# Kernel optimization log

Hardware: AMD Instinct MI355X
Metric: run time of the kernel (lower is better)

Reference implementation:

```python
import jax, jax.numpy as jnp
import numpy as np

B, S, D, H, HD, NF, NL, V = 16, 2048, 768, 12, 64, 32, 12, 2362
EPS = 1e-6  # fast_transformers LinearAttention eps


def _rope_tables(seq_len, dim):
    inv_freq = 1.0 / (10000.0 ** (jnp.arange(0, dim, 2, dtype=jnp.float32) / dim))
    t = jnp.arange(seq_len, dtype=jnp.float32)
    freqs = jnp.einsum('s,f->sf', t, inv_freq)
    emb = jnp.concatenate([freqs, freqs], axis=-1)[None, :, None, :]  # [1,S,1,HD]
    return jnp.cos(emb), jnp.sin(emb)


def _rot_half(x):
    x1, x2 = jnp.split(x, 2, axis=-1)
    return jnp.concatenate([-x2, x1], axis=-1)


def _ln(x, g, b):
    m = jnp.mean(x, axis=-1, keepdims=True)
    v = jnp.var(x, axis=-1, keepdims=True)
    return (x - m) / jnp.sqrt(v + 1e-5) * g + b


def setup_inputs():
    key = jax.random.key(0)
    ks = jax.random.split(key, 16)
    w = lambda k, shape: jax.random.normal(k, shape, jnp.float32) * 0.02
    return {
        'idx': jax.random.randint(ks[0], (B, S), 0, V),
        'mask': jnp.ones((B, S), jnp.int32),
        'emb': w(ks[1], (V, D)),
        'wq': w(ks[2], (NL, D, D)), 'bq': jnp.zeros((NL, D), jnp.float32),
        'wk': w(ks[3], (NL, D, D)), 'bk': jnp.zeros((NL, D), jnp.float32),
        'wv': w(ks[4], (NL, D, D)), 'bv': jnp.zeros((NL, D), jnp.float32),
        'wo': w(ks[5], (NL, D, D)), 'bo': jnp.zeros((NL, D), jnp.float32),
        'omega': jax.random.normal(ks[6], (NL, HD, NF), jnp.float32),
        'g1': jnp.ones((NL, D), jnp.float32), 'be1': jnp.zeros((NL, D), jnp.float32),
        'w1': w(ks[7], (NL, D, D)), 'c1': jnp.zeros((NL, D), jnp.float32),
        'w2': w(ks[8], (NL, D, D)), 'c2': jnp.zeros((NL, D), jnp.float32),
        'g2': jnp.ones((NL, D), jnp.float32), 'be2': jnp.zeros((NL, D), jnp.float32),
        'gf': jnp.ones((D,), jnp.float32), 'bf': jnp.zeros((D,), jnp.float32),
    }


def reference(idx, mask, emb, wq, bq, wk, bk, wv, bv, wo, bo, omega,
              g1, be1, w1, c1, w2, c2, g2, be2, gf, bf):
    x = emb[idx]                     # token embedding [B,S,D]; dropout = identity (eval)
    m = mask.astype(x.dtype)         # LengthMask from mask.sum(-1); mask is contiguous ones
    cos, sin = _rope_tables(S, HD)
    for l in range(NL):
        q = (x @ wq[l] + bq[l]).reshape(B, S, H, HD)
        k = (x @ wk[l] + bk[l]).reshape(B, S, H, HD)
        v = (x @ wv[l] + bv[l]).reshape(B, S, H, HD)
        q = q * cos + _rot_half(q) * sin
        k = k * cos + _rot_half(k) * sin
        # GeneralizedRandomFeatures: phi(x) = relu(x @ omega)
        Qf = jax.nn.relu(jnp.einsum('bshd,df->bshf', q, omega[l]))
        Kf = jax.nn.relu(jnp.einsum('bshd,df->bshf', k, omega[l])) * m[:, :, None, None]
        KV = jnp.einsum('bshf,bshd->bhfd', Kf, v)                       # [B,H,NF,HD]
        Z = 1.0 / (jnp.einsum('bshf,bhf->bsh', Qf, Kf.sum(axis=1)) + EPS)
        a = jnp.einsum('bshf,bhfd,bsh->bshd', Qf, KV, Z).reshape(B, S, D)
        x = x + (a @ wo[l] + bo[l])           # residual (dropout=identity)
        x = _ln(x, g1[l], be1[l])             # post-norm
        y = jax.nn.gelu(x @ w1[l] + c1[l], approximate=False) @ w2[l] + c2[l]
        x = _ln(x + y, g2[l], be2[l])
    return _ln(x, gf, bf)                     # final encoder LayerNorm
```

## Files before the change

kernel.cpp:

```cpp
#include <hip/hip_runtime.h>
#include <cstdint>
#include <cstddef>

typedef __bf16 bf16;
typedef __bf16 bf16x8 __attribute__((ext_vector_type(8)));
typedef __bf16 bf16x4 __attribute__((ext_vector_type(4)));
typedef float f32x4 __attribute__((ext_vector_type(4)));

#define NB 16
#define SS 2048
#define HH 12
#define NLL 12
#define MTOK (NB*SS)

#define BARRIER() do { asm volatile("" ::: "memory"); __builtin_amdgcn_s_barrier(); asm volatile("" ::: "memory"); } while (0)
#define VMCNT0()  asm volatile("s_waitcnt vmcnt(0)" ::: "memory")

__device__ __forceinline__ void load16_lds(const bf16* g, bf16* l) {
    __builtin_amdgcn_global_load_lds((const __attribute__((address_space(1))) void*)g,
                                     (__attribute__((address_space(3))) void*)l, 16, 0, 0);
}

__global__ void diag_k(float* out, float code) {
    if (threadIdx.x == 0 && blockIdx.x == 0) out[0] = code;
}

__global__ __launch_bounds__(256) void packw_k(const float* __restrict__ wq, const float* __restrict__ wk,
                                               const float* __restrict__ wv, const float* __restrict__ wo,
                                               const float* __restrict__ w1, const float* __restrict__ w2,
                                               int l, bf16* qkvT_l, bf16* oT_l, bf16* w1T_l, bf16* w2T_l) {
    __shared__ float tile[32][33];
    int which = blockIdx.z;
    const float* srcs[6] = {wq, wk, wv, wo, w1, w2};
    const float* src = srcs[which] + (size_t)l * 589824;
    bf16* dst;
    if (which < 3)       dst = qkvT_l + (size_t)which * 589824;
    else if (which == 3) dst = oT_l;
    else if (which == 4) dst = w1T_l;
    else                 dst = w2T_l;
    int tx = threadIdx.x, ty = threadIdx.y;
    int bx = blockIdx.x, by = blockIdx.y;
#pragma unroll
    for (int j = 0; j < 4; ++j)
        tile[ty + j*8][tx] = src[(size_t)(by*32 + ty + j*8) * 768 + bx*32 + tx];
    __syncthreads();
#pragma unroll
    for (int j = 0; j < 4; ++j)
        dst[(size_t)(bx*32 + ty + j*8) * 768 + by*32 + tx] = (bf16)tile[tx][ty + j*8];
}

__global__ void packb_k(const float* __restrict__ bq, const float* __restrict__ bk,
                        const float* __restrict__ bv, float* bqkv) {
    int i = blockIdx.x * 256 + threadIdx.x;
    if (i >= NLL * 2304) return;
    int l = i / 2304, c = i % 2304;
    float v = (c < 768) ? bq[l*768 + c] : (c < 1536) ? bk[l*768 + c - 768] : bv[l*768 + c - 1536];
    bqkv[i] = v;
}

__global__ void rope_k(float* cosT, float* sinT) {
    int i = blockIdx.x * 256 + threadIdx.x;
    int s = i >> 6, j = i & 63, f = j & 31;
    float inv = powf(10000.f, -(float)(2*f) * (1.0f/64.0f));
    float ang = (float)s * inv;
    cosT[i] = cosf(ang);
    sinT[i] = sinf(ang);
}

__global__ __launch_bounds__(192) void embed_k(const int* __restrict__ idx, const float* __restrict__ emb,
                                               float* __restrict__ x, bf16* __restrict__ xb) {
    size_t tok = blockIdx.x;
    int t = threadIdx.x;
    int id = idx[tok];
    float4 v = *(const float4*)&emb[(size_t)id * 768 + t*4];
    *(float4*)&x[tok * 768 + t*4] = v;
    bf16x4 o; o[0] = (bf16)v.x; o[1] = (bf16)v.y; o[2] = (bf16)v.z; o[3] = (bf16)v.w;
    *(bf16x4*)&xb[tok * 768 + t*4] = o;
}

__global__ __launch_bounds__(512, 4)
void gemmqkv_k(const bf16* __restrict__ A, const bf16* __restrict__ Bt,
               const float* __restrict__ bias, bf16* __restrict__ outb, int N) {
    const int K = 768;
    __shared__ bf16 sh[24576];
    const int t = threadIdx.x;
    const int w = t >> 6, lane = t & 63;
    const int wr = w >> 1, wc = w & 1;

    const int nx = gridDim.x;
    const int L = blockIdx.y * nx + blockIdx.x;
    const int xcd = L & 7, bi = L >> 3;
    const int bcol = (bi % nx) * 128;
    const int brow = ((bi / nx) * 8 + xcd) * 256;

    const int srow = t >> 2;
    const int scol = (((t & 3) * 16) ^ (((srow >> 1) & 3) << 4)) >> 1;

    auto stageA = [&](int s, int k0) {
        load16_lds(A + (size_t)(brow + srow)       * K + k0 + scol, &sh[s*8192 + t*8]);
        load16_lds(A + (size_t)(brow + 128 + srow) * K + k0 + scol, &sh[s*8192 + 4096 + t*8]);
    };
    auto stageB = [&](int s, int k0) {
        load16_lds(Bt + (size_t)(bcol + srow)      * K + k0 + scol, &sh[16384 + s*4096 + t*8]);
    };

    const int rowa = lane & 15, kg = lane >> 4;
    const int celem = ((kg * 16) ^ (((rowa >> 1) & 3) << 4)) >> 1;

    f32x4  acc[4][4] = {};
    bf16x8 af[4], bg[4];

    stageA(0, 0); stageB(0, 0);
    VMCNT0();
    BARRIER();

    for (int kt = 0; kt < 24; ++kt) {
        const int cur = kt & 1, nb = cur ^ 1;
        const int kn = (kt + 1) * 32;
        const bool st = (kt < 23);
#pragma unroll
        for (int mi = 0; mi < 4; ++mi)
            af[mi] = *(const bf16x8*)&sh[cur*8192 + (wr*64 + mi*16 + rowa)*32 + celem];
#pragma unroll
        for (int ni = 0; ni < 4; ++ni)
            bg[ni] = *(const bf16x8*)&sh[16384 + cur*4096 + (wc*64 + ni*16 + rowa)*32 + celem];
        if (st) { stageA(nb, kn); stageB(nb, kn); }
        BARRIER();
        __builtin_amdgcn_s_setprio(1);
#pragma unroll
        for (int mi = 0; mi < 4; ++mi)
#pragma unroll
            for (int ni = 0; ni < 4; ++ni)
                acc[mi][ni] = __builtin_amdgcn_mfma_f32_16x16x32_bf16(af[mi], bg[ni], acc[mi][ni], 0, 0, 0);
        __builtin_amdgcn_s_setprio(0);
        VMCNT0();
        BARRIER();
    }

    bf16* Cs = sh;
    const int r0 = (lane >> 4) * 4, c0 = lane & 15;
    const int ch = t & 7, rr = t >> 3;
#pragma unroll
    for (int h = 0; h < 2; ++h) {
        __syncthreads();
        if (wc == h) {
#pragma unroll
            for (int mi = 0; mi < 4; ++mi)
#pragma unroll
                for (int ni = 0; ni < 4; ++ni) {
                    int col = bcol + wc * 64 + ni * 16 + c0;
                    float bv = bias[col];
#pragma unroll
                    for (int r = 0; r < 4; ++r)
                        Cs[(wr*64 + mi*16 + r0 + r) * 64 + ni*16 + c0] =
                            (bf16)(acc[mi][ni][r] + bv);
                }
        }
        __syncthreads();
#pragma unroll
        for (int i = 0; i < 4; ++i) {
            int row = rr + i * 64;
            *(bf16x8*)&outb[(size_t)(brow + row) * N + bcol + h*64 + ch*8] =
                *(const bf16x8*)&Cs[row * 64 + ch * 8];
        }
    }
}

template <int MODE>
__global__ __launch_bounds__(256)
void gemm128_k(const bf16* __restrict__ A, const bf16* __restrict__ Bt,
               const float* __restrict__ bias, bf16* __restrict__ outb, int N) {
    const int K = 768;
    __shared__ bf16 sh[16384];
    bf16* As = sh;
    bf16* Bs = sh + 8192;
    const int t = threadIdx.x;
    const int w = t >> 6, lane = t & 63;
    const int wr = w >> 1, wc = w & 1;

    const int nx = gridDim.x;
    const int L = blockIdx.y * nx + blockIdx.x;
    const int xcd = L & 7, bi = L >> 3;
    const int bcol = (bi % nx) * 128;
    const int brow = ((bi / nx) * 8 + xcd) * 128;

    const int srow = t >> 3;
    const int scol = (((t & 7) * 16) ^ ((srow & 7) << 4)) >> 1;
    const int rowa = lane & 15, kg = lane >> 4;
    const int rsw  = (rowa & 7) << 4;

    f32x4 acc[4][4] = {};

    for (int k0 = 0; k0 < K; k0 += 64) {
        __syncthreads();
#pragma unroll
        for (int j = 0; j < 4; ++j) {
            load16_lds(A  + (size_t)(brow + j*32 + srow) * K + k0 + scol, &As[j*2048 + t*8]);
            load16_lds(Bt + (size_t)(bcol + j*32 + srow) * K + k0 + scol, &Bs[j*2048 + t*8]);
        }
        __syncthreads();
        bf16x8 af[4][2], bg[4][2];
#pragma unroll
        for (int mi = 0; mi < 4; ++mi)
#pragma unroll
            for (int ks = 0; ks < 2; ++ks)
                af[mi][ks] = *(const bf16x8*)&As[(wr*64 + mi*16 + rowa)*64 + (((ks*64 + kg*16) ^ rsw) >> 1)];
#pragma unroll
        for (int ni = 0; ni < 4; ++ni)
#pragma unroll
            for (int ks = 0; ks < 2; ++ks)
                bg[ni][ks] = *(const bf16x8*)&Bs[(wc*64 + ni*16 + rowa)*64 + (((ks*64 + kg*16) ^ rsw) >> 1)];
#pragma unroll
        for (int mi = 0; mi < 4; ++mi)
#pragma unroll
            for (int ni = 0; ni < 4; ++ni)
#pragma unroll
                for (int ks = 0; ks < 2; ++ks)
                    acc[mi][ni] = __builtin_amdgcn_mfma_f32_16x16x32_bf16(af[mi][ks], bg[ni][ks], acc[mi][ni], 0, 0, 0);
    }

    __syncthreads();
    const int r0 = (lane >> 4) * 4, c0 = lane & 15;
#pragma unroll
    for (int mi = 0; mi < 4; ++mi)
#pragma unroll
        for (int ni = 0; ni < 4; ++ni) {
            int col = bcol + wc * 64 + ni * 16 + c0;
            float bv = bias[col];
#pragma unroll
            for (int r = 0; r < 4; ++r) {
                float v = acc[mi][ni][r] + bv;
                if (MODE == 1) v = 0.5f * v * (1.f + erff(v * 0.70710678118f));
                sh[(wr*64 + mi*16 + r0 + r) * 128 + wc*64 + ni*16 + c0] = (bf16)v;
            }
        }
    __syncthreads();
    const int ch = t & 15, rr = t >> 4;
#pragma unroll
    for (int i = 0; i < 8; ++i) {
        int row = rr + i * 16;
        *(bf16x8*)&outb[(size_t)(brow + row) * N + bcol + ch*8] =
            *(const bf16x8*)&sh[row * 128 + ch * 8];
    }
}

__global__ __launch_bounds__(192) void phi_k(const bf16* __restrict__ qkv, const float* __restrict__ cosT,
                                             const float* __restrict__ sinT, const float* __restrict__ omega_l,
                                             const int* __restrict__ mask, bf16* __restrict__ Qf,
                                             bf16* __restrict__ Kf) {
    __shared__ float roped[2][4][12][65];
    __shared__ float om[64][32];
    int t = threadIdx.x;
    size_t tok0 = (size_t)blockIdx.x * 4;

    for (int i = t; i < 2048; i += 192) ((float*)om)[i] = omega_l[i];

    {
        int side = t / 96, cr = t % 96, h = cr >> 3, cq = cr & 7;
        float sgn = (cq < 4) ? -1.f : 1.f;
        for (int it = 0; it < 4; ++it) {
            size_t tokg = tok0 + it;
            int s = (int)(tokg & (SS - 1));
            const bf16* rowp = qkv + tokg * 2304 + side * 768 + h * 64;
            bf16x8 mv = *(const bf16x8*)(rowp + cq * 8);
            bf16x8 pv = *(const bf16x8*)(rowp + (cq ^ 4) * 8);
            const float* cp = cosT + s * 64 + cq * 8;
            const float* sp = sinT + s * 64 + cq * 8;
#pragma unroll
            for (int e = 0; e < 8; ++e) {
                float r = (float)mv[e] * cp[e] + sgn * (float)pv[e] * sp[e];
                roped[side][it][h][cq * 8 + e] = r;
            }
        }
    }
    __syncthreads();

    int side = t / 96, rr = t % 96, h = rr >> 3, f0 = (rr & 7) * 4;
    float acc[4][4] = {};
    for (int d = 0; d < 64; ++d) {
        float4 o = *(const float4*)&om[d][f0];
#pragma unroll
        for (int tk = 0; tk < 4; ++tk) {
            float qv = roped[side][tk][h][d];
            acc[tk][0] += qv * o.x; acc[tk][1] += qv * o.y;
            acc[tk][2] += qv * o.z; acc[tk][3] += qv * o.w;
        }
    }
    bf16* outb = (side == 0) ? Qf : Kf;
#pragma unroll
    for (int tk = 0; tk < 4; ++tk) {
        size_t tokg = tok0 + tk;
        float m = (side == 1) ? (float)mask[tokg] : 1.f;
        bf16x4 v;
        v[0] = (bf16)(fmaxf(acc[tk][0], 0.f) * m);
        v[1] = (bf16)(fmaxf(acc[tk][1], 0.f) * m);
        v[2] = (bf16)(fmaxf(acc[tk][2], 0.f) * m);
        v[3] = (bf16)(fmaxf(acc[tk][3], 0.f) * m);
        *(bf16x4*)&outb[(tokg * 12 + h) * 32 + f0] = v;
    }
}

__global__ __launch_bounds__(256) void kvp_k(const bf16* __restrict__ Kf, const bf16* __restrict__ qkv,
                                             float* __restrict__ KVp, float* __restrict__ Ksp) {
    int ch = blockIdx.x, h = blockIdx.y, b = blockIdx.z;
    __shared__ float kts[64][32];
    __shared__ bf16 vts[64][64];
    int t = threadIdx.x;
    int fg = t & 15, dg = t >> 4;
    int f0 = fg * 2, d0 = dg * 4;
    float acc[8] = {};
    float ksm[2] = {};
    for (int s0 = ch * 256; s0 < ch * 256 + 256; s0 += 64) {
        __syncthreads();
        {
            int row = t >> 2, slot = t & 3;
            bf16x8 k8 = *(const bf16x8*)&Kf[((size_t)(b * SS + s0 + row) * 12 + h) * 32 + slot * 8];
#pragma unroll
            for (int e = 0; e < 8; ++e) kts[row][slot * 8 + e] = (float)k8[e];
            int c0 = t, c1 = t + 256;
            *(float4*)&vts[c0 >> 3][(c0 & 7) * 8] =
                *(const float4*)&qkv[(size_t)(b * SS + s0 + (c0 >> 3)) * 2304 + 1536 + h * 64 + (c0 & 7) * 8];
            *(float4*)&vts[c1 >> 3][(c1 & 7) * 8] =
                *(const float4*)&qkv[(size_t)(b * SS + s0 + (c1 >> 3)) * 2304 + 1536 + h * 64 + (c1 & 7) * 8];
        }
        __syncthreads();
#pragma unroll 4
        for (int sl = 0; sl < 64; ++sl) {
            float2 kk = *(const float2*)&kts[sl][f0];
            bf16x4 vv = *(const bf16x4*)&vts[sl][d0];
            float v0 = (float)vv[0], v1 = (float)vv[1], v2 = (float)vv[2], v3 = (float)vv[3];
            acc[0] += kk.x * v0; acc[1] += kk.x * v1; acc[2] += kk.x * v2; acc[3] += kk.x * v3;
            acc[4] += kk.y * v0; acc[5] += kk.y * v1; acc[6] += kk.y * v2; acc[7] += kk.y * v3;
            if (dg == 0) { ksm[0] += kk.x; ksm[1] += kk.y; }
        }
    }
    size_t base = (((size_t)(b * 12 + h) * 8 + ch) * 32) * 64;
#pragma unroll
    for (int i = 0; i < 2; ++i)
#pragma unroll
        for (int j = 0; j < 4; ++j)
            KVp[base + (size_t)(f0 + i) * 64 + d0 + j] = acc[i * 4 + j];
    if (dg == 0) {
        size_t kb = ((size_t)(b * 12 + h) * 8 + ch) * 32;
        Ksp[kb + f0] = ksm[0]; Ksp[kb + f0 + 1] = ksm[1];
    }
}

__global__ __launch_bounds__(256) void kvc_k(const float* __restrict__ KVp, const float* __restrict__ Ksp,
                                             float* __restrict__ KV, float* __restrict__ Ksum) {
    int bh = blockIdx.x, t = threadIdx.x;
    size_t base = (size_t)bh * 8 * 2048;
    float v[8] = {};
    for (int ch = 0; ch < 8; ++ch)
#pragma unroll
        for (int j = 0; j < 8; ++j) v[j] += KVp[base + (size_t)ch * 2048 + t * 8 + j];
#pragma unroll
    for (int j = 0; j < 8; ++j) KV[(size_t)bh * 2048 + t * 8 + j] = v[j];
    if (t < 32) {
        float s = 0.f;
        for (int ch = 0; ch < 8; ++ch) s += Ksp[((size_t)bh * 8 + ch) * 32 + t];
        Ksum[(size_t)bh * 32 + t] = s;
    }
}

__global__ __launch_bounds__(256) void comb_k(const bf16* __restrict__ Qf, const float* __restrict__ KV,
                                              const float* __restrict__ Ksum, bf16* __restrict__ aout) {
    int ch = blockIdx.x, h = blockIdx.y, b = blockIdx.z;
    int bh = b * 12 + h;
    int t = threadIdx.x, sl = t >> 6, d = t & 63;
    const float* kvb = KV + (size_t)bh * 2048;
    const float* ksb = Ksum + (size_t)bh * 32;
    float kvcol[32], ksr[32];
#pragma unroll
    for (int f = 0; f < 32; ++f) kvcol[f] = kvb[f * 64 + d];
#pragma unroll
    for (int f = 0; f < 32; ++f) ksr[f] = ksb[f];
    for (int g = 0; g < 16; ++g) {
        int s = ch * 64 + g * 4 + sl;
        size_t tok = (size_t)b * SS + s;
        const bf16* qf = Qf + (tok * 12 + h) * 32;
        float accd = 0.f, accz = 0.f;
#pragma unroll
        for (int fb = 0; fb < 4; ++fb) {
            bf16x8 q8 = *(const bf16x8*)(qf + fb * 8);
#pragma unroll
            for (int e = 0; e < 8; ++e) {
                float q = (float)q8[e];
                accd += q * kvcol[fb * 8 + e];
                accz += q * ksr[fb * 8 + e];
            }
        }
        float z = 1.f / (accz + 1e-6f);
        aout[tok * 768 + h * 64 + d] = (bf16)(accd * z);
    }
}

__global__ __launch_bounds__(192) void ln2_k(const float* xsrc, const bf16* ysrc,
                                             const float* __restrict__ g, const float* __restrict__ be,
                                             float* xout, bf16* xbout) {
    size_t tok = blockIdx.x;
    int t = threadIdx.x;
    float4 v = *(const float4*)&xsrc[tok * 768 + t * 4];
    if (ysrc) {
        bf16x4 yv = *(const bf16x4*)&ysrc[tok * 768 + t * 4];
        v.x += (float)yv[0]; v.y += (float)yv[1]; v.z += (float)yv[2]; v.w += (float)yv[3];
    }
    float s = v.x + v.y + v.z + v.w;
    float q = v.x * v.x + v.y * v.y + v.z * v.z + v.w * v.w;
#pragma unroll
    for (int off = 32; off > 0; off >>= 1) { s += __shfl_down(s, off); q += __shfl_down(q, off); }
    __shared__ float sred[3], qred[3];
    int w = t >> 6, lane = t & 63;
    if (lane == 0) { sred[w] = s; qred[w] = q; }
    __syncthreads();
    s = sred[0] + sred[1] + sred[2];
    q = qred[0] + qred[1] + qred[2];
    float mean = s * (1.f / 768.f);
    float var = q * (1.f / 768.f) - mean * mean;
    float inv = rsqrtf(var + 1e-5f);
    float4 gg = *(const float4*)&g[t * 4];
    float4 bb = *(const float4*)&be[t * 4];
    float4 o;
    o.x = (v.x - mean) * inv * gg.x + bb.x;
    o.y = (v.y - mean) * inv * gg.y + bb.y;
    o.z = (v.z - mean) * inv * gg.z + bb.z;
    o.w = (v.w - mean) * inv * gg.w + bb.w;
    *(float4*)&xout[tok * 768 + t * 4] = o;
    if (xbout) {
        bf16x4 ob; ob[0] = (bf16)o.x; ob[1] = (bf16)o.y; ob[2] = (bf16)o.z; ob[3] = (bf16)o.w;
        *(bf16x4*)&xbout[tok * 768 + t * 4] = ob;
    }
}

extern "C" void kernel_launch(void* const* d_in, const int* in_sizes, int n_in,
                              void* d_out, int out_size, void* d_ws, size_t ws_size,
                              hipStream_t stream) {
    const int*   idx   = (const int*)d_in[0];
    const int*   mask  = (const int*)d_in[1];
    const float* emb   = (const float*)d_in[2];
    const float* wq    = (const float*)d_in[3];
    const float* bq    = (const float*)d_in[4];
    const float* wk    = (const float*)d_in[5];
    const float* bk    = (const float*)d_in[6];
    const float* wv    = (const float*)d_in[7];
    const float* bv    = (const float*)d_in[8];
    const float* wo    = (const float*)d_in[9];
    const float* bo    = (const float*)d_in[10];
    const float* omega = (const float*)d_in[11];
    const float* g1    = (const float*)d_in[12];
    const float* be1   = (const float*)d_in[13];
    const float* w1    = (const float*)d_in[14];
    const float* c1    = (const float*)d_in[15];
    const float* w2    = (const float*)d_in[16];
    const float* c2    = (const float*)d_in[17];
    const float* g2    = (const float*)d_in[18];
    const float* be2   = (const float*)d_in[19];
    const float* gf    = (const float*)d_in[20];
    const float* bff   = (const float*)d_in[21];
    float* dout = (float*)d_out;

    char* wsb = (char*)d_ws;
    size_t off = 0;
    auto nxt = [&](size_t bytes) -> void* {
        void* p = wsb + off;
        off += bytes;
        off = (off + 255) & ~(size_t)255;
        return p;
    };

    float* cosT  = (float*)nxt((size_t)SS * 64 * 4);
    float* sinT  = (float*)nxt((size_t)SS * 64 * 4);
    bf16*  qkvTl = (bf16*)nxt((size_t)2304 * 768 * 2);
    bf16*  oTl   = (bf16*)nxt((size_t)768 * 768 * 2);
    bf16*  w1Tl  = (bf16*)nxt((size_t)768 * 768 * 2);
    bf16*  w2Tl  = (bf16*)nxt((size_t)768 * 768 * 2);
    float* bqkv  = (float*)nxt((size_t)NLL * 2304 * 4);
    float* x     = (float*)nxt((size_t)MTOK * 768 * 4);
    bf16*  xb    = (bf16*)nxt((size_t)MTOK * 768 * 2);
    bf16*  qkv   = (bf16*)nxt((size_t)MTOK * 2304 * 2);
    bf16*  Qf    = (bf16*)nxt((size_t)MTOK * 384 * 2);
    bf16*  Kf    = (bf16*)nxt((size_t)MTOK * 384 * 2);
    float* KVp   = (float*)nxt((size_t)NB * HH * 8 * 2048 * 4);
    float* Ksp   = (float*)nxt((size_t)NB * HH * 8 * 32 * 4);
    float* KV    = (float*)nxt((size_t)NB * HH * 2048 * 4);
    float* Ksum  = (float*)nxt((size_t)NB * HH * 32 * 4);
    size_t needed = off;

    if (ws_size < needed) {
        diag_k<<<dim3(1), dim3(64), 0, stream>>>(dout, 10000.f + (float)(ws_size >> 20));
        return;
    }

    bf16* abuf = qkv;
    bf16* h1   = (bf16*)((char*)qkv + (size_t)MTOK * 768 * 2);
    bf16* y    = (bf16*)((char*)qkv + (size_t)MTOK * 768 * 4);

    packb_k<<<dim3((NLL * 2304 + 255) / 256), dim3(256), 0, stream>>>(bq, bk, bv, bqkv);
    rope_k<<<dim3(SS * 64 / 256), dim3(256), 0, stream>>>(cosT, sinT);
    embed_k<<<dim3(MTOK), dim3(192), 0, stream>>>(idx, emb, x, xb);

    for (int l = 0; l < NLL; ++l) {
        const float* bqkv_l = bqkv + (size_t)l * 2304;
        const float* om_l   = omega + (size_t)l * 2048;

        packw_k<<<dim3(24, 24, 6), dim3(32, 8), 0, stream>>>(wq, wk, wv, wo, w1, w2, l, qkvTl, oTl, w1Tl, w2Tl);
        gemmqkv_k<<<dim3(18, 128), dim3(512), 0, stream>>>(xb, qkvTl, bqkv_l, qkv, 2304);
        phi_k<<<dim3(MTOK / 4), dim3(192), 0, stream>>>(qkv, cosT, sinT, om_l, mask, Qf, Kf);
        kvp_k<<<dim3(8, HH, NB), dim3(256), 0, stream>>>(Kf, qkv, KVp, Ksp);
        kvc_k<<<dim3(NB * HH), dim3(256), 0, stream>>>(KVp, Ksp, KV, Ksum);
        comb_k<<<dim3(32, HH, NB), dim3(256), 0, stream>>>(Qf, KV, Ksum, abuf);
        gemm128_k<0><<<dim3(6, 256), dim3(256), 0, stream>>>(abuf, oTl, bo + (size_t)l * 768, y, 768);
        ln2_k<<<dim3(MTOK), dim3(192), 0, stream>>>(x, y, g1 + (size_t)l * 768, be1 + (size_t)l * 768, x, xb);
        gemm128_k<1><<<dim3(6, 256), dim3(256), 0, stream>>>(xb, w1Tl, c1 + (size_t)l * 768, h1, 768);
        gemm128_k<0><<<dim3(6, 256), dim3(256), 0, stream>>>(h1, w2Tl, c2 + (size_t)l * 768, y, 768);
        ln2_k<<<dim3(MTOK), dim3(192), 0, stream>>>(x, y, g2 + (size_t)l * 768, be2 + (size_t)l * 768, x,
                                                    (l == NLL - 1) ? nullptr : xb);
    }
    ln2_k<<<dim3(MTOK), dim3(192), 0, stream>>>(x, nullptr, gf, bff, dout, nullptr);
}
```

Measured before the change: 7.296 ms.

## Fuse RoPE and random-feature projection into the QKV GEMM epilogue

```diff
diff --git a/kernel.cpp b/kernel.cpp
--- a/kernel.cpp
+++ b/kernel.cpp
@@ -80,7 +80,10 @@
 
 __global__ __launch_bounds__(512, 4)
 void gemmqkv_k(const bf16* __restrict__ A, const bf16* __restrict__ Bt,
-               const float* __restrict__ bias, bf16* __restrict__ outb, int N) {
+               const float* __restrict__ bias,
+               const float* __restrict__ cosT, const float* __restrict__ sinT,
+               const float* __restrict__ omega_l, const int* __restrict__ mask,
+               bf16* __restrict__ vout, bf16* __restrict__ Qf, bf16* __restrict__ Kf, int N) {
     const int K = 768;
     __shared__ bf16 sh[24576];
     const int t = threadIdx.x;
@@ -137,32 +140,111 @@
         BARRIER();
     }
 
-    bf16* Cs = sh;
     const int r0 = (lane >> 4) * 4, c0 = lane & 15;
-    const int ch = t & 7, rr = t >> 3;
-#pragma unroll
+
+    if (bcol >= 1536) {
+        bf16* Cs = sh;
+        const int ch = t & 7, rr = t >> 3;
+#pragma unroll
+        for (int h = 0; h < 2; ++h) {
+            __syncthreads();
+            if (wc == h) {
+#pragma unroll
+                for (int mi = 0; mi < 4; ++mi)
+#pragma unroll
+                    for (int ni = 0; ni < 4; ++ni) {
+                        int col = bcol + wc * 64 + ni * 16 + c0;
+                        float bv = bias[col];
+#pragma unroll
+                        for (int r = 0; r < 4; ++r)
+                            Cs[(wr*64 + mi*16 + r0 + r) * 64 + ni*16 + c0] =
+                                (bf16)(acc[mi][ni][r] + bv);
+                    }
+            }
+            __syncthreads();
+#pragma unroll
+            for (int i = 0; i < 4; ++i) {
+                int row = rr + i * 64;
+                *(bf16x8*)&vout[(size_t)(brow + row) * N + bcol + h*64 + ch*8] =
+                    *(const bf16x8*)&Cs[row * 64 + ch * 8];
+            }
+        }
+        return;
+    }
+
+    const int side = (bcol >= 768) ? 1 : 0;
+    const int head0 = (bcol - side * 768) >> 6;
+    bf16* Cs  = sh;
+    bf16* omT = sh + 16384;
+
+    __syncthreads();
+    for (int i = t; i < 2048; i += 512) {
+        int f = i >> 6, d = i & 63;
+        int byte = f * 128 + ((d * 2) ^ ((f & 7) << 4));
+        *(bf16*)((char*)omT + byte) = (bf16)omega_l[d * 32 + f];
+    }
+
+    const int rsw2 = (rowa & 7) << 4;
+    bf16* outp = side ? Kf : Qf;
+
+#pragma unroll 1
     for (int h = 0; h < 2; ++h) {
         __syncthreads();
         if (wc == h) {
+            float bv[4];
+#pragma unroll
+            for (int ni = 0; ni < 4; ++ni) bv[ni] = bias[bcol + h*64 + ni*16 + c0];
 #pragma unroll
             for (int mi = 0; mi < 4; ++mi)
 #pragma unroll
-                for (int ni = 0; ni < 4; ++ni) {
-                    int col = bcol + wc * 64 + ni * 16 + c0;
-                    float bv = bias[col];
-#pragma unroll
-                    for (int r = 0; r < 4; ++r)
-                        Cs[(wr*64 + mi*16 + r0 + r) * 64 + ni*16 + c0] =
-                            (bf16)(acc[mi][ni][r] + bv);
+                for (int r = 0; r < 4; ++r) {
+                    int row = wr*64 + mi*16 + r0 + r;
+                    int s = (brow + row) & (SS - 1);
+                    const float* cp = cosT + s*64;
+                    const float* sp = sinT + s*64;
+                    float q[4];
+#pragma unroll
+                    for (int ni = 0; ni < 4; ++ni) q[ni] = acc[mi][ni][r] + bv[ni];
+#pragma unroll
+                    for (int ni = 0; ni < 4; ++ni) {
+                        int d = ni*16 + c0;
+                        float rv = q[ni]*cp[d] + (ni < 2 ? -q[ni^2] : q[ni^2]) * sp[d];
+                        int byte = row*128 + ((d*2) ^ ((row & 7) << 4));
+                        *(bf16*)((char*)Cs + byte) = (bf16)rv;
+                    }
                 }
         }
         __syncthreads();
-#pragma unroll
-        for (int i = 0; i < 4; ++i) {
-            int row = rr + i * 64;
-            *(bf16x8*)&outb[(size_t)(brow + row) * N + bcol + h*64 + ch*8] =
-                *(const bf16x8*)&Cs[row * 64 + ch * 8];
-        }
+        f32x4 pac[2][2] = {};
+#pragma unroll
+        for (int ks = 0; ks < 2; ++ks) {
+            const int cb = ks*64 + kg*16;
+            bf16x8 paf[2], pbg[2];
+#pragma unroll
+            for (int j = 0; j < 2; ++j)
+                paf[j] = *(const bf16x8*)&Cs[((w*2 + j)*16 + rowa)*64 + ((cb ^ rsw2) >> 1)];
+#pragma unroll
+            for (int ft = 0; ft < 2; ++ft)
+                pbg[ft] = *(const bf16x8*)&omT[(ft*16 + rowa)*64 + ((cb ^ rsw2) >> 1)];
+#pragma unroll
+            for (int j = 0; j < 2; ++j)
+#pragma unroll
+                for (int ft = 0; ft < 2; ++ft)
+                    pac[j][ft] = __builtin_amdgcn_mfma_f32_16x16x32_bf16(paf[j], pbg[ft], pac[j][ft], 0, 0, 0);
+        }
+        const int head = head0 + h;
+#pragma unroll
+        for (int j = 0; j < 2; ++j)
+#pragma unroll
+            for (int r = 0; r < 4; ++r) {
+                size_t tok = (size_t)brow + (w*2 + j)*16 + r0 + r;
+                float m = side ? (float)mask[tok] : 1.f;
+#pragma unroll
+                for (int ft = 0; ft < 2; ++ft) {
+                    float v = fmaxf(pac[j][ft][r], 0.f) * m;
+                    outp[(tok*12 + head)*32 + ft*16 + c0] = (bf16)v;
+                }
+            }
     }
 }
 
@@ -241,62 +323,6 @@
         int row = rr + i * 16;
         *(bf16x8*)&outb[(size_t)(brow + row) * N + bcol + ch*8] =
             *(const bf16x8*)&sh[row * 128 + ch * 8];
-    }
-}
-
-__global__ __launch_bounds__(192) void phi_k(const bf16* __restrict__ qkv, const float* __restrict__ cosT,
-                                             const float* __restrict__ sinT, const float* __restrict__ omega_l,
-                                             const int* __restrict__ mask, bf16* __restrict__ Qf,
-                                             bf16* __restrict__ Kf) {
-    __shared__ float roped[2][4][12][65];
-    __shared__ float om[64][32];
-    int t = threadIdx.x;
-    size_t tok0 = (size_t)blockIdx.x * 4;
-
-    for (int i = t; i < 2048; i += 192) ((float*)om)[i] = omega_l[i];
-
-    {
-        int side = t / 96, cr = t % 96, h = cr >> 3, cq = cr & 7;
-        float sgn = (cq < 4) ? -1.f : 1.f;
-        for (int it = 0; it < 4; ++it) {
-            size_t tokg = tok0 + it;
-            int s = (int)(tokg & (SS - 1));
-            const bf16* rowp = qkv + tokg * 2304 + side * 768 + h * 64;
-            bf16x8 mv = *(const bf16x8*)(rowp + cq * 8);
-            bf16x8 pv = *(const bf16x8*)(rowp + (cq ^ 4) * 8);
-            const float* cp = cosT + s * 64 + cq * 8;
-            const float* sp = sinT + s * 64 + cq * 8;
-#pragma unroll
-            for (int e = 0; e < 8; ++e) {
-                float r = (float)mv[e] * cp[e] + sgn * (float)pv[e] * sp[e];
-                roped[side][it][h][cq * 8 + e] = r;
-            }
-        }
-    }
-    __syncthreads();
-
-    int side = t / 96, rr = t % 96, h = rr >> 3, f0 = (rr & 7) * 4;
-    float acc[4][4] = {};
-    for (int d = 0; d < 64; ++d) {
-        float4 o = *(const float4*)&om[d][f0];
-#pragma unroll
-        for (int tk = 0; tk < 4; ++tk) {
-            float qv = roped[side][tk][h][d];
-            acc[tk][0] += qv * o.x; acc[tk][1] += qv * o.y;
-            acc[tk][2] += qv * o.z; acc[tk][3] += qv * o.w;
-        }
-    }
-    bf16* outb = (side == 0) ? Qf : Kf;
-#pragma unroll
-    for (int tk = 0; tk < 4; ++tk) {
-        size_t tokg = tok0 + tk;
-        float m = (side == 1) ? (float)mask[tokg] : 1.f;
-        bf16x4 v;
-        v[0] = (bf16)(fmaxf(acc[tk][0], 0.f) * m);
-        v[1] = (bf16)(fmaxf(acc[tk][1], 0.f) * m);
-        v[2] = (bf16)(fmaxf(acc[tk][2], 0.f) * m);
-        v[3] = (bf16)(fmaxf(acc[tk][3], 0.f) * m);
-        *(bf16x4*)&outb[(tokg * 12 + h) * 32 + f0] = v;
     }
 }
 
@@ -504,8 +530,8 @@
         const float* om_l   = omega + (size_t)l * 2048;
 
         packw_k<<<dim3(24, 24, 6), dim3(32, 8), 0, stream>>>(wq, wk, wv, wo, w1, w2, l, qkvTl, oTl, w1Tl, w2Tl);
-        gemmqkv_k<<<dim3(18, 128), dim3(512), 0, stream>>>(xb, qkvTl, bqkv_l, qkv, 2304);
-        phi_k<<<dim3(MTOK / 4), dim3(192), 0, stream>>>(qkv, cosT, sinT, om_l, mask, Qf, Kf);
+        gemmqkv_k<<<dim3(18, 128), dim3(512), 0, stream>>>(xb, qkvTl, bqkv_l, cosT, sinT, om_l, mask,
+                                                           qkv, Qf, Kf, 2304);
         kvp_k<<<dim3(8, HH, NB), dim3(256), 0, stream>>>(Kf, qkv, KVp, Ksp);
         kvc_k<<<dim3(NB * HH), dim3(256), 0, stream>>>(KVp, Ksp, KV, Ksum);
         comb_k<<<dim3(32, HH, NB), dim3(256), 0, stream>>>(Qf, KV, Ksum, abuf);
```

Result: slower. 11.02 ms (+51.1%).
